# Optimization experiments

Measured on AMD Instinct MI355X. Metric: run time of the kernel, lower is better.

The kernel has to match this reference:

```python
import jax, jax.numpy as jnp
import numpy as np


def setup_inputs() -> dict:
    key = jax.random.key(0)
    k1, k2, k3, k4 = jax.random.split(key, 4)
    B, Nq, Nc, D = 4, 1024, 16384, 1024
    return {
        "query_embeddings": jax.random.normal(k1, (B, Nq, D), dtype=jnp.float32),
        "context_embeddings": jax.random.normal(k2, (B, Nc, D), dtype=jnp.float32),
        "W": jax.random.normal(k3, (D, D), dtype=jnp.float32) * (1.0 / np.sqrt(D)),
        "b": jax.random.normal(k4, (D,), dtype=jnp.float32) * 0.02,
    }


TOP_N = 5


def _pairwise_l2(q, c):
    # q: [B, Nq, D], c: [B, Nc, D] -> [B, Nq, Nc] Euclidean distances
    q_sq = jnp.sum(q * q, axis=-1, keepdims=True)          # [B, Nq, 1]
    c_sq = jnp.sum(c * c, axis=-1)[:, None, :]             # [B, 1, Nc]
    cross = jnp.einsum("bqd,bcd->bqc", q, c)               # [B, Nq, Nc]
    d2 = jnp.maximum(q_sq + c_sq - 2.0 * cross, 0.0)
    return jnp.sqrt(d2)


def reference(query_embeddings, context_embeddings, W, b):
    # latent query projection (nn.Linear): x @ W.T + b
    q_proj = jnp.einsum("bqd,ed->bqe", query_embeddings, W) + b
    distances = _pairwise_l2(q_proj, context_embeddings)    # [B, Nq, Nc]
    # smallest top_n distances -> top_k on negated values
    neg_d, idx = jax.lax.top_k(-distances, TOP_N)
    return (-neg_d, idx)
```

## Files before the change

### kernel.cpp

```cpp
#include <hip/hip_runtime.h>
#include <cfloat>
#include <math.h>

#define D_DIM 1024
#define B_DIM 4
#define NQ    1024
#define NC    16384
#define TOPN  5
#define TOPA  5
#define CSPLIT 8
#define CAND  (TOPA*CSPLIT)
#define QT    64
#define CTILE 256
#define BK    64

#define PBM 128
#define PBN 64
#define PBK 32
#define PPAD 4
#define PROJ_BLKS ((D_DIM/PBN) * ((B_DIM*NQ)/PBM))

typedef __bf16 bf16x8 __attribute__((ext_vector_type(8)));
typedef float  f32x4  __attribute__((ext_vector_type(4)));
typedef double f64x4  __attribute__((ext_vector_type(4)));

__device__ __forceinline__ unsigned short f2bf(float f) {
    unsigned u = __builtin_bit_cast(unsigned, f);
    unsigned r = (u + 0x7fffu + ((u >> 16) & 1u)) >> 16;
    return (unsigned short)r;
}

__device__ __forceinline__ void gload16(const void* g, void* l) {
    __builtin_amdgcn_global_load_lds(
        (const __attribute__((address_space(1))) unsigned*)g,
        (__attribute__((address_space(3))) unsigned*)l, 16, 0, 0);
}

template<int N, typename T>
__device__ __forceinline__ void topk_insert(T (&bv)[N], int (&bi)[N], T v, int ci) {
    if (v < bv[N-1] || (v == bv[N-1] && ci < bi[N-1])) {
        bv[N-1] = v; bi[N-1] = ci;
        #pragma unroll
        for (int s = N-1; s > 0; --s) {
            bool sw = (bv[s] < bv[s-1]) || (bv[s] == bv[s-1] && bi[s] < bi[s-1]);
            if (sw) {
                T tv = bv[s-1]; bv[s-1] = bv[s]; bv[s] = tv;
                int ti = bi[s-1]; bi[s-1] = bi[s]; bi[s] = ti;
            }
        }
    }
}

template<int N>
__device__ __forceinline__ void insN(float (&bv)[N], int (&bi)[N], float v, int ci) {
    if (v < bv[N-1]) {
        bv[N-1] = v; bi[N-1] = ci;
        #pragma unroll
        for (int s = N-1; s > 0; --s) {
            if (bv[s] < bv[s-1]) {
                float tv = bv[s-1]; bv[s-1] = bv[s]; bv[s] = tv;
                int   ti = bi[s-1]; bi[s-1] = bi[s]; bi[s] = ti;
            }
        }
    }
}

__device__ __forceinline__ void ins5b(float (&bv)[TOPA], int (&bi)[TOPA], float v, int ci) {
    #pragma unroll
    for (int s = 0; s < TOPA; ++s) {
        const bool  c    = v < bv[s];
        const float vmin = c ? v : bv[s];
        const float vmax = c ? bv[s] : v;
        const int   imin = c ? ci : bi[s];
        const int   imax = c ? bi[s] : ci;
        bv[s] = vmin; bi[s] = imin;
        v = vmax; ci = imax;
    }
}

__global__ __launch_bounds__(256) void proj_packc_kernel(const float* __restrict__ Q,
                                                         const float* __restrict__ W,
                                                         const float* __restrict__ bias,
                                                         const float* __restrict__ C,
                                                         double* __restrict__ P64,
                                                         unsigned short* __restrict__ Pbf,
                                                         float* __restrict__ qsq,
                                                         unsigned short* __restrict__ Cbf,
                                                         float* __restrict__ csq)
{
    const int bid = blockIdx.x;
    if (bid >= PROJ_BLKS) {
        int wave = threadIdx.x >> 6;
        int lane = threadIdx.x & 63;
        int row  = (bid - PROJ_BLKS) * 4 + wave;
        const float* x = C + (size_t)row * D_DIM;
        float s = 0.f;
        #pragma unroll
        for (int i = 0; i < 4; ++i) {
            float4 v = *(const float4*)&x[lane * 4 + i * 256];
            s += v.x * v.x + v.y * v.y + v.z * v.z + v.w * v.w;
            ushort4 h;
            h.x = f2bf(v.x); h.y = f2bf(v.y); h.z = f2bf(v.z); h.w = f2bf(v.w);
            *(ushort4*)&Cbf[(size_t)row * D_DIM + lane * 4 + i * 256] = h;
        }
        #pragma unroll
        for (int off = 32; off; off >>= 1) s += __shfl_down(s, off, 64);
        if (lane == 0) csq[row] = s;
        return;
    }
    __shared__ __align__(16) float Qs[PBM][PBK + PPAD];
    __shared__ __align__(16) float Ws[PBN][PBK + PPAD];

    const int t    = threadIdx.x;
    const int lane = t & 63;
    const int w    = t >> 6;
    const int l15  = lane & 15;
    const int l4   = lane >> 4;
    const int m0   = (bid >> 4) * PBM;
    const int n0   = (bid & 15) * PBN;
    const int wm   = (w >> 1) * 64;
    const int wn   = (w & 1) * 32;

    const int srow = t >> 3;
    const int scol = (t & 7) * 4;

    f64x4 acc[4][2];
    #pragma unroll
    for (int fm = 0; fm < 4; ++fm)
        #pragma unroll
        for (int fn = 0; fn < 2; ++fn) acc[fm][fn] = (f64x4)0.0;

    for (int k0 = 0; k0 < D_DIM; k0 += PBK) {
        float4 qa0 = *(const float4*)&Q[(size_t)(m0 + srow)      * D_DIM + k0 + scol];
        float4 qa1 = *(const float4*)&Q[(size_t)(m0 + srow + 32) * D_DIM + k0 + scol];
        float4 qa2 = *(const float4*)&Q[(size_t)(m0 + srow + 64) * D_DIM + k0 + scol];
        float4 qa3 = *(const float4*)&Q[(size_t)(m0 + srow + 96) * D_DIM + k0 + scol];
        float4 wa0 = *(const float4*)&W[(size_t)(n0 + srow)      * D_DIM + k0 + scol];
        float4 wa1 = *(const float4*)&W[(size_t)(n0 + srow + 32) * D_DIM + k0 + scol];
        __syncthreads();
        *(float4*)&Qs[srow][scol]      = qa0;
        *(float4*)&Qs[srow + 32][scol] = qa1;
        *(float4*)&Qs[srow + 64][scol] = qa2;
        *(float4*)&Qs[srow + 96][scol] = qa3;
        *(float4*)&Ws[srow][scol]      = wa0;
        *(float4*)&Ws[srow + 32][scol] = wa1;
        __syncthreads();

        #pragma unroll
        for (int ks = 0; ks < PBK / 4; ++ks) {
            const int kc = ks * 4 + l4;
            double a[4], b[2];
            #pragma unroll
            for (int fm = 0; fm < 4; ++fm) a[fm] = (double)Qs[wm + fm * 16 + l15][kc];
            #pragma unroll
            for (int fn = 0; fn < 2; ++fn) b[fn] = (double)Ws[wn + fn * 16 + l15][kc];
            #pragma unroll
            for (int fm = 0; fm < 4; ++fm)
                #pragma unroll
                for (int fn = 0; fn < 2; ++fn)
                    acc[fm][fn] = __builtin_amdgcn_mfma_f64_16x16x4f64(a[fm], b[fn], acc[fm][fn], 0, 0, 0);
        }
    }

    #pragma unroll
    for (int fm = 0; fm < 4; ++fm) {
        #pragma unroll
        for (int j = 0; j < 4; ++j) {
            const int row = m0 + wm + fm * 16 + j * 4 + l4;
            float part = 0.f;
            #pragma unroll
            for (int fn = 0; fn < 2; ++fn) {
                const int col = n0 + wn + fn * 16 + l15;
                double d = acc[fm][fn][j] + (double)bias[col];
                P64[(size_t)row * D_DIM + col] = d;
                float a = (float)d;
                part += a * a;
                Pbf[(size_t)row * D_DIM + col] = f2bf(a);
            }
            #pragma unroll
            for (int m = 1; m < 16; m <<= 1) part += __shfl_xor(part, m, 64);
            if (l15 == 0) atomicAdd(&qsq[row], part);
        }
    }
}

__global__ __launch_bounds__(256) void perm_detect_kernel(const float* __restrict__ Q,
                                                          const float* __restrict__ W,
                                                          const float* __restrict__ bias,
                                                          const double* __restrict__ P64,
                                                          int* __restrict__ invperm)
{
    __shared__ double tv[16];
    const int t = threadIdx.x;
    const int g = t >> 4;
    const int s = t & 15;
    if (t < 16) invperm[t] = t;

    double acc = 0.0;
    const int kb = s * 64;
    for (int k = 0; k < 64; ++k)
        acc = fma((double)Q[(size_t)g * D_DIM + kb + k], (double)W[kb + k], acc);
    #pragma unroll
    for (int off = 8; off; off >>= 1) acc += __shfl_down(acc, off, 16);
    if (s == 0) tv[g] = acc + (double)bias[0];
    __syncthreads();

    if (t < 16) {
        double p = P64[(size_t)t * D_DIM];
        int best = 0; double bd = fabs(p - tv[0]);
        #pragma unroll
        for (int i = 1; i < 16; ++i) {
            double d = fabs(p - tv[i]);
            if (d < bd) { bd = d; best = i; }
        }
        invperm[best] = t;
    }
}

__global__ __launch_bounds__(256, 3) void dist_mfma_kernel(const unsigned short* __restrict__ Pbf,
                                                           const unsigned short* __restrict__ Cbf,
                                                           const float* __restrict__ qsq,
                                                           const float* __restrict__ csq,
                                                           int* __restrict__ pi)
{
    __shared__ __align__(16) short CsS[CTILE * 64];
    __shared__ __align__(16) short QsS[QT * 64];
    float* MV = (float*)CsS;
    int*   MI = (int*)(CsS + 4096);

    const int t    = threadIdx.x;
    const int lane = t & 63;
    const int w    = t >> 6;
    const int l15  = lane & 15;
    const int l4   = lane >> 4;
    const int r8   = lane >> 3;
    const int sc   = lane & 7;
    const int csplit = blockIdx.x;
    const int by = blockIdx.y;
    const int bz = blockIdx.z;
    const int qg0 = bz * NQ + by * QT;

    unsigned cOff[8], qOff[2];
    #pragma unroll
    for (int j = 0; j < 8; ++j)
        cOff[j] = (unsigned)((w * 64 + j * 8 + r8) * D_DIM + (sc ^ r8) * 8);
    #pragma unroll
    for (int j = 0; j < 2; ++j)
        qOff[j] = (unsigned)((w * 16 + j * 8 + r8) * D_DIM + (sc ^ r8) * 8);

    float qsv[4];
    #pragma unroll
    for (int s = 0; s < 4; ++s) qsv[s] = qsq[qg0 + s * 16 + l15];

    float bv[4][TOPA]; int bi[4][TOPA];
    #pragma unroll
    for (int s = 0; s < 4; ++s)
        #pragma unroll
        for (int j = 0; j < TOPA; ++j) { bv[s][j] = FLT_MAX; bi[s][j] = 0x7fffffff; }

    const int cpb = NC / CSPLIT;
    for (int it = 0; it < cpb / CTILE; ++it) {
        const int cg0 = csplit * cpb + it * CTILE;
        const size_t crow0 = (size_t)bz * NC + cg0;

        f32x4 acc[4][4];
        #pragma unroll
        for (int u = 0; u < 4; ++u)
            #pragma unroll
            for (int s = 0; s < 4; ++s) acc[u][s] = (f32x4)0.0f;

        for (int k0 = 0; k0 < D_DIM; k0 += BK) {
            const unsigned short* cB = Cbf + crow0 * D_DIM + k0;
            const unsigned short* qB = Pbf + (size_t)qg0 * D_DIM + k0;
            __syncthreads();
            #pragma unroll
            for (int j = 0; j < 8; ++j)
                gload16(cB + cOff[j], &CsS[(w * 64 + j * 8) * 64]);
            #pragma unroll
            for (int j = 0; j < 2; ++j)
                gload16(qB + qOff[j], &QsS[(w * 16 + j * 8) * 64]);
            __syncthreads();
            #pragma unroll
            for (int ks = 0; ks < 2; ++ks) {
                const int sp = ((ks * 4 + l4) ^ (l15 & 7)) * 8;
                bf16x8 bq[4], ac[4];
                #pragma unroll
                for (int s = 0; s < 4; ++s)
                    bq[s] = *(const bf16x8*)&QsS[(s * 16 + l15) * 64 + sp];
                #pragma unroll
                for (int u = 0; u < 4; ++u)
                    ac[u] = *(const bf16x8*)&CsS[(w * 64 + u * 16 + l15) * 64 + sp];
                #pragma unroll
                for (int u = 0; u < 4; ++u)
                    #pragma unroll
                    for (int s = 0; s < 4; ++s)
                        acc[u][s] = __builtin_amdgcn_mfma_f32_16x16x32_bf16(ac[u], bq[s], acc[u][s], 0, 0, 0);
            }
        }

        #pragma unroll
        for (int u = 0; u < 4; ++u) {
            const int crow = w * 64 + u * 16 + l4 * 4;
            float4 cs4 = *(const float4*)&csq[(size_t)bz * NC + cg0 + crow];
            float csa[4] = {cs4.x, cs4.y, cs4.z, cs4.w};
            #pragma unroll
            for (int s = 0; s < 4; ++s) {
                #pragma unroll
                for (int r = 0; r < 4; ++r) {
                    float v = qsv[s] + csa[r] - 2.0f * acc[u][s][r];
                    ins5b(bv[s], bi[s], v, cg0 + crow + r);
                }
            }
        }
    }

    #pragma unroll
    for (int mask = 16; mask <= 32; mask <<= 1) {
        #pragma unroll
        for (int s = 0; s < 4; ++s) {
            float ov[TOPA]; int oi[TOPA];
            #pragma unroll
            for (int j = 0; j < TOPA; ++j) {
                ov[j] = __shfl_xor(bv[s][j], mask, 64);
                oi[j] = __shfl_xor(bi[s][j], mask, 64);
            }
            #pragma unroll
            for (int j = 0; j < TOPA; ++j) insN<TOPA>(bv[s], bi[s], ov[j], oi[j]);
        }
    }
    __syncthreads();
    if (l4 == 0) {
        #pragma unroll
        for (int s = 0; s < 4; ++s) {
            int q = s * 16 + l15;
            #pragma unroll
            for (int j = 0; j < TOPA; ++j) {
                MV[(q * 4 + w) * TOPA + j] = bv[s][j];
                MI[(q * 4 + w) * TOPA + j] = bi[s][j];
            }
        }
    }
    __syncthreads();
    if (t < QT) {
        float mv[TOPA]; int mi[TOPA];
        #pragma unroll
        for (int j = 0; j < TOPA; ++j) { mv[j] = FLT_MAX; mi[j] = 0x7fffffff; }
        for (int l = 0; l < 4; ++l)
            #pragma unroll
            for (int j = 0; j < TOPA; ++j)
                insN<TOPA>(mv, mi, MV[(t * 4 + l) * TOPA + j], MI[(t * 4 + l) * TOPA + j]);
        size_t base = (((size_t)qg0 + t) * CSPLIT + csplit) * TOPA;
        #pragma unroll
        for (int j = 0; j < TOPA; ++j) pi[base + j] = mi[j];
    }
}

__global__ __launch_bounds__(256) void refine_kernel(const double* __restrict__ P64,
                                                     const int* __restrict__ invperm,
                                                     const float* __restrict__ C,
                                                     const int*   __restrict__ pi,
                                                     float* __restrict__ out)
{
    __shared__ double pS[D_DIM];
    __shared__ double dvs[CAND];
    __shared__ int    dis[CAND];
    const int q    = blockIdx.x;
    const int pq   = (q & ~15) | invperm[q & 15];
    const int bz   = q >> 10;
    const int t    = threadIdx.x;
    const int wave = t >> 6;
    const int lane = t & 63;
    const double* p = P64 + (size_t)pq * D_DIM;

    #pragma unroll
    for (int j = 0; j < D_DIM / 256; ++j) pS[t + j * 256] = p[t + j * 256];
    __syncthreads();

    for (int k = wave; k < CAND; k += 4) {
        int ci = pi[(size_t)pq * CAND + k];
        const float* c = C + ((size_t)bz * NC + ci) * D_DIM;
        double s = 0.0;
        #pragma unroll
        for (int j = 0; j < 16; ++j) {
            int d = lane + 64 * j;
            double diff = pS[d] - (double)c[d];
            s = fma(diff, diff, s);
        }
        #pragma unroll
        for (int off = 32; off; off >>= 1) s += __shfl_down(s, off, 64);
        if (lane == 0) { dvs[k] = s; dis[k] = ci; }
    }
    __syncthreads();
    if (t == 0) {
        double bv[TOPN]; int bi[TOPN];
        #pragma unroll
        for (int j = 0; j < TOPN; ++j) { bv[j] = DBL_MAX; bi[j] = 0x7fffffff; }
        for (int k = 0; k < CAND; ++k)
            topk_insert<TOPN,double>(bv, bi, dvs[k], dis[k]);
        #pragma unroll
        for (int j = 0; j < TOPN; ++j) {
            out[(size_t)q * TOPN + j] = (float)sqrt(bv[j]);
            out[(size_t)B_DIM * NQ * TOPN + (size_t)q * TOPN + j] = (float)bi[j];
        }
    }
}

extern "C" void kernel_launch(void* const* d_in, const int* in_sizes, int n_in,
                              void* d_out, int out_size, void* d_ws, size_t ws_size,
                              hipStream_t stream) {
    const float* Q    = (const float*)d_in[0];
    const float* C    = (const float*)d_in[1];
    const float* W    = (const float*)d_in[2];
    const float* bias = (const float*)d_in[3];
    float* out = (float*)d_out;

    char* ws = (char*)d_ws;
    double*         P64 = (double*)ws;
    unsigned short* Pbf = (unsigned short*)(ws + (size_t)32 * 1024 * 1024);
    unsigned short* Cbf = (unsigned short*)(ws + (size_t)40 * 1024 * 1024);
    float*          qsq = (float*)(ws + (size_t)168 * 1024 * 1024);
    float*          csq = qsq + 4096;
    int*            pi  = (int*)(csq + 65536);
    int*            ivp = pi + (size_t)B_DIM * NQ * CAND;

    hipMemsetAsync(qsq, 0, (size_t)B_DIM * NQ * sizeof(float), stream);
    proj_packc_kernel<<<PROJ_BLKS + (B_DIM * NC) / 4, 256, 0, stream>>>(Q, W, bias, C, P64, Pbf, qsq, Cbf, csq);
    perm_detect_kernel<<<1, 256, 0, stream>>>(Q, W, bias, P64, ivp);
    dist_mfma_kernel<<<dim3(CSPLIT, NQ / QT, B_DIM), 256, 0, stream>>>(Pbf, Cbf, qsq, csq, pi);
    refine_kernel<<<B_DIM * NQ, 256, 0, stream>>>(P64, ivp, C, pi, out);
}
```

Baseline: 857.6 us.

## Double-buffer LDS tiles in distance kernel to overlap global loads with MFMA

```diff
diff --git a/kernel.cpp b/kernel.cpp
--- a/kernel.cpp
+++ b/kernel.cpp
@@ -13,6 +13,7 @@
 #define QT    64
 #define CTILE 256
 #define BK    64
+#define NSTEP (D_DIM/BK)
 
 #define PBM 128
 #define PBN 64
@@ -217,16 +218,16 @@
     }
 }
 
-__global__ __launch_bounds__(256, 3) void dist_mfma_kernel(const unsigned short* __restrict__ Pbf,
+__global__ __launch_bounds__(256, 2) void dist_mfma_kernel(const unsigned short* __restrict__ Pbf,
                                                            const unsigned short* __restrict__ Cbf,
                                                            const float* __restrict__ qsq,
                                                            const float* __restrict__ csq,
                                                            int* __restrict__ pi)
 {
-    __shared__ __align__(16) short CsS[CTILE * 64];
-    __shared__ __align__(16) short QsS[QT * 64];
-    float* MV = (float*)CsS;
-    int*   MI = (int*)(CsS + 4096);
+    __shared__ __align__(16) short CsS[2][CTILE * 64];
+    __shared__ __align__(16) short QsS[2][QT * 64];
+    float* MV = (float*)&CsS[0][0];
+    int*   MI = (int*)&CsS[0][4096];
 
     const int t    = threadIdx.x;
     const int lane = t & 63;
@@ -239,6 +240,9 @@
     const int by = blockIdx.y;
     const int bz = blockIdx.z;
     const int qg0 = bz * NQ + by * QT;
+    const int cpb = NC / CSPLIT;
+    const int cgb = csplit * cpb;
+    const int nIt = cpb / CTILE;
 
     unsigned cOff[8], qOff[2];
     #pragma unroll
@@ -248,6 +252,9 @@
     for (int j = 0; j < 2; ++j)
         qOff[j] = (unsigned)((w * 16 + j * 8 + r8) * D_DIM + (sc ^ r8) * 8);
 
+    const unsigned short* cBase = Cbf + ((size_t)bz * NC + cgb) * D_DIM;
+    const unsigned short* qBase = Pbf + (size_t)qg0 * D_DIM;
+
     float qsv[4];
     #pragma unroll
     for (int s = 0; s < 4; ++s) qsv[s] = qsq[qg0 + s * 16 + l15];
@@ -258,10 +265,22 @@
         #pragma unroll
         for (int j = 0; j < TOPA; ++j) { bv[s][j] = FLT_MAX; bi[s][j] = 0x7fffffff; }
 
-    const int cpb = NC / CSPLIT;
-    for (int it = 0; it < cpb / CTILE; ++it) {
-        const int cg0 = csplit * cpb + it * CTILE;
-        const size_t crow0 = (size_t)bz * NC + cg0;
+    auto stage = [&](int it, int kk, int b) {
+        const unsigned short* cB = cBase + (size_t)(it * CTILE) * D_DIM + kk * BK;
+        const unsigned short* qB = qBase + kk * BK;
+        #pragma unroll
+        for (int j = 0; j < 8; ++j)
+            gload16(cB + cOff[j], &CsS[b][(w * 64 + j * 8) * 64]);
+        #pragma unroll
+        for (int j = 0; j < 2; ++j)
+            gload16(qB + qOff[j], &QsS[b][(w * 16 + j * 8) * 64]);
+    };
+
+    stage(0, 0, 0);
+    int cur = 0;
+
+    for (int it = 0; it < nIt; ++it) {
+        const int cg0 = cgb + it * CTILE;
 
         f32x4 acc[4][4];
         #pragma unroll
@@ -269,33 +288,35 @@
             #pragma unroll
             for (int s = 0; s < 4; ++s) acc[u][s] = (f32x4)0.0f;
 
-        for (int k0 = 0; k0 < D_DIM; k0 += BK) {
-            const unsigned short* cB = Cbf + crow0 * D_DIM + k0;
-            const unsigned short* qB = Pbf + (size_t)qg0 * D_DIM + k0;
-            __syncthreads();
-            #pragma unroll
-            for (int j = 0; j < 8; ++j)
-                gload16(cB + cOff[j], &CsS[(w * 64 + j * 8) * 64]);
-            #pragma unroll
-            for (int j = 0; j < 2; ++j)
-                gload16(qB + qOff[j], &QsS[(w * 16 + j * 8) * 64]);
-            __syncthreads();
+        for (int kk = 0; kk < NSTEP; ++kk) {
+            if (it == nIt - 1 && kk == NSTEP - 1) {
+                __builtin_amdgcn_sched_barrier(0);
+                asm volatile("s_waitcnt vmcnt(0)\n\ts_barrier" ::: "memory");
+            } else {
+                int nk = kk + 1, nit = it;
+                if (nk == NSTEP) { nk = 0; ++nit; }
+                stage(nit, nk, cur ^ 1);
+                __builtin_amdgcn_sched_barrier(0);
+                asm volatile("s_waitcnt vmcnt(10)\n\ts_barrier" ::: "memory");
+            }
             #pragma unroll
             for (int ks = 0; ks < 2; ++ks) {
                 const int sp = ((ks * 4 + l4) ^ (l15 & 7)) * 8;
                 bf16x8 bq[4], ac[4];
                 #pragma unroll
                 for (int s = 0; s < 4; ++s)
-                    bq[s] = *(const bf16x8*)&QsS[(s * 16 + l15) * 64 + sp];
+                    bq[s] = *(const bf16x8*)&QsS[cur][(s * 16 + l15) * 64 + sp];
                 #pragma unroll
                 for (int u = 0; u < 4; ++u)
-                    ac[u] = *(const bf16x8*)&CsS[(w * 64 + u * 16 + l15) * 64 + sp];
+                    ac[u] = *(const bf16x8*)&CsS[cur][(w * 64 + u * 16 + l15) * 64 + sp];
                 #pragma unroll
                 for (int u = 0; u < 4; ++u)
                     #pragma unroll
                     for (int s = 0; s < 4; ++s)
                         acc[u][s] = __builtin_amdgcn_mfma_f32_16x16x32_bf16(ac[u], bq[s], acc[u][s], 0, 0, 0);
             }
+            asm volatile("s_barrier" ::: "memory");
+            cur ^= 1;
         }
 
         #pragma unroll
```

After: 851.0 us. No clear change (-0.8%).
